# Optimization experiments

Hardware: AMD Instinct MI355X
Metric: run time of the kernel (lower is better)

## Reference

```python
import jax, jax.numpy as jnp
import numpy as np

COMMIT = 0.25
DECAY = 0.999
EPS = 1e-05


def setup_inputs() -> dict:
    key = jax.random.key(0)
    k1, k2, k3, k4 = jax.random.split(key, 4)
    N, M, D = 8, 512, 32
    B, H, W = 32, 32, 32
    return {
        "x": jax.random.normal(k1, (B, N * D, H, W), jnp.float32),
        "embedding": jax.random.uniform(k2, (N, M, D), jnp.float32, -1.0 / M, 1.0 / M),
        "ema_count": jax.random.uniform(k3, (N, M), jnp.float32),
        "ema_weight": jax.random.normal(k4, (N, M, D), jnp.float32) * (1.0 / M),
    }


def reference(x, embedding, ema_count, ema_weight):
    B, C, H, W = x.shape
    N, M, D = embedding.shape  # C == N * D
    xr = x.reshape(B, N, D, H, W).transpose(1, 0, 3, 4, 2)  # [N,B,H,W,D]
    L = B * H * W
    x_flat = jax.lax.stop_gradient(xr).reshape(N, L, D)  # [N,L,D]

    e2 = jnp.sum(embedding ** 2, axis=2)[:, None, :]          # [N,1,M]
    x2 = jnp.sum(x_flat ** 2, axis=2, keepdims=True)          # [N,L,1]
    distances = e2 + x2 - 2.0 * jnp.einsum('nld,nmd->nlm', x_flat, embedding)

    indices = jnp.argmin(distances, axis=-1)                  # [N,L]
    quantized = jnp.take_along_axis(embedding, indices[:, :, None], axis=1)  # [N,L,D]
    quantized = jax.lax.stop_gradient(quantized).reshape(xr.shape)

    # one-hot count / encodings^T @ x_flat expressed as scatter-adds
    n_idx = jnp.arange(N)[:, None]
    counts = jnp.zeros((N, M), x.dtype).at[n_idx, indices].add(1.0)         # [N,M]
    dw = jnp.zeros((N, M, D), x.dtype).at[n_idx, indices].add(x_flat)       # [N,M,D]

    # EMA codebook update (training branch)
    ema_count_new = DECAY * ema_count + (1.0 - DECAY) * counts
    n_tot = jnp.sum(ema_count_new, axis=-1, keepdims=True)
    ema_count_new = (ema_count_new + EPS) / (n_tot + M * EPS) * n_tot
    ema_weight_new = DECAY * ema_weight + (1.0 - DECAY) * dw
    embedding_new = ema_weight_new / ema_count_new[..., None]

    e_latent_loss = jnp.mean((xr - quantized) ** 2)
    loss = COMMIT * e_latent_loss

    quantized_st = xr + jax.lax.stop_gradient(quantized - xr)  # straight-through
    out = quantized_st.transpose(1, 0, 4, 2, 3).reshape(B, C, H, W)

    avg_probs = counts / L                                     # mean of one-hot encodings
    perplexity = jnp.exp(-jnp.sum(avg_probs * jnp.log(avg_probs + 1e-10), axis=-1))

    return out, loss, perplexity.sum(), embedding_new, ema_count_new, ema_weight_new
```

## Files before the change

kernel.cpp:

```cpp
#include <hip/hip_runtime.h>
#include <cfloat>
#include <cmath>

#define NB 32
#define NN 8
#define NM 512
#define ND 32
#define NHW 1024
#define NC 256
#define NCHW (NC * NHW)
#define NL (NB * NHW)
#define EPAD 40
#define XPAD 33

static constexpr float DECAYF = (float)0.999;
static constexpr float OMDF = (float)(1.0 - 0.999);
static constexpr float EPSF = 1e-5f;
static constexpr float MEPSF = (float)(512.0 * 1e-5);
static constexpr float LOSS_SCALE = (float)(0.25 / 8388608.0);

#define OUT_LOSS (NB * NC * NHW)
#define OUT_PERP (OUT_LOSS + 1)
#define OUT_EMB (OUT_PERP + 1)
#define OUT_CNT (OUT_EMB + NN * NM * ND)
#define OUT_W (OUT_CNT + NN * NM)

typedef __attribute__((ext_vector_type(8))) short bf16x8;
typedef __attribute__((ext_vector_type(4))) float f32x4;

__device__ inline unsigned short f2bf(float f) {
    unsigned u = __builtin_bit_cast(unsigned, f);
    u += 0x7FFFu + ((u >> 16) & 1u);
    return (unsigned short)(u >> 16);
}
__device__ inline float bf2f(unsigned short h) {
    unsigned u = ((unsigned)h) << 16;
    return __builtin_bit_cast(float, u);
}

__global__ void e_prep(const float* __restrict__ emb, unsigned short* __restrict__ ehi,
                       unsigned short* __restrict__ elo, float* __restrict__ e2) {
    const int i = blockIdx.x * 256 + threadIdx.x;
    const float* e = emb + i * ND;
    unsigned short* hi = ehi + (size_t)i * EPAD;
    unsigned short* lo = elo + (size_t)i * EPAD;
    float s = 0.f;
#pragma unroll
    for (int d = 0; d < ND; ++d) {
        const float v = e[d];
        s = fmaf(v, v, s);
        const unsigned short h = f2bf(v);
        hi[d] = h;
        lo[d] = f2bf(v - bf2f(h));
    }
    e2[i] = s;
}

__launch_bounds__(256, 2)
__global__ void vq_argmin(const float* __restrict__ x,
                          const unsigned short* __restrict__ ehi,
                          const unsigned short* __restrict__ elo,
                          const float* __restrict__ e2g,
                          const float* __restrict__ emb,
                          float* __restrict__ out,
                          unsigned short* __restrict__ idx_out,
                          float* __restrict__ loss_out) {
    __shared__ __align__(16) unsigned short shi[256 * EPAD];
    __shared__ __align__(16) unsigned short slo[256 * EPAD];
    __shared__ float se2[NM];
    __shared__ __align__(16) float sx[256 * XPAD];
    __shared__ unsigned short sidx[256];
    __shared__ float red[4];

    const int n = blockIdx.y;
    const int lbase = blockIdx.x * 256;
    const int tid = threadIdx.x;
    const int b = lbase >> 10;
    const int hw0 = lbase & (NHW - 1);

    {
        const float* xp = x + (size_t)b * NCHW + n * ND * NHW + hw0 + tid;
#pragma unroll
        for (int d = 0; d < ND; ++d)
            sx[tid * XPAD + d] = xp[d * NHW];
    }
    for (int i = tid; i < NM; i += 256) se2[i] = e2g[n * NM + i];
    __syncthreads();

    const int lane = tid & 63;
    const int w = tid >> 6;
    const int j16 = lane & 15;
    const int kg = lane >> 4;

    bf16x8 ah[4], al[4];
#pragma unroll
    for (int lt = 0; lt < 4; ++lt) {
        const int row = w * 64 + lt * 16 + j16;
        const float* sr = &sx[row * XPAD + kg * 8];
#pragma unroll
        for (int j = 0; j < 8; ++j) {
            const float v = sr[j];
            const unsigned short h = f2bf(v);
            ah[lt][j] = (short)h;
            al[lt][j] = (short)f2bf(v - bf2f(h));
        }
    }

    float bd[4][4];
    int bm[4][4];
#pragma unroll
    for (int lt = 0; lt < 4; ++lt)
#pragma unroll
        for (int r = 0; r < 4; ++r) { bd[lt][r] = FLT_MAX; bm[lt][r] = 0; }

    for (int half = 0; half < 2; ++half) {
        __syncthreads();
        {
            const unsigned* srch = (const unsigned*)(ehi + ((size_t)n * NM + half * 256) * EPAD);
            const unsigned* srcl = (const unsigned*)(elo + ((size_t)n * NM + half * 256) * EPAD);
            unsigned* dsth = (unsigned*)shi;
            unsigned* dstl = (unsigned*)slo;
            for (int i = tid; i < 256 * EPAD / 2; i += 256) {
                dsth[i] = srch[i];
                dstl[i] = srcl[i];
            }
        }
        __syncthreads();

        for (int mt = 0; mt < 16; ++mt) {
            const int mloc = mt * 16 + j16;
            const bf16x8 bh = *(const bf16x8*)&shi[mloc * EPAD + kg * 8];
            const bf16x8 bl = *(const bf16x8*)&slo[mloc * EPAD + kg * 8];
            const int mglob = half * 256 + mloc;
            const float e2v = se2[mglob];
#pragma unroll
            for (int lt = 0; lt < 4; ++lt) {
                f32x4 c = {0.f, 0.f, 0.f, 0.f};
                c = __builtin_amdgcn_mfma_f32_16x16x32_bf16(ah[lt], bh, c, 0, 0, 0);
                c = __builtin_amdgcn_mfma_f32_16x16x32_bf16(al[lt], bh, c, 0, 0, 0);
                c = __builtin_amdgcn_mfma_f32_16x16x32_bf16(ah[lt], bl, c, 0, 0, 0);
#pragma unroll
                for (int r = 0; r < 4; ++r) {
                    const float dist = fmaf(-2.f, c[r], e2v);
                    if (dist < bd[lt][r]) { bd[lt][r] = dist; bm[lt][r] = mglob; }
                }
            }
        }
    }

#pragma unroll
    for (int lt = 0; lt < 4; ++lt)
#pragma unroll
        for (int r = 0; r < 4; ++r) {
            float d0 = bd[lt][r];
            int m0 = bm[lt][r];
#pragma unroll
            for (int off = 1; off < 16; off <<= 1) {
                const float dn = __shfl_xor(d0, off, 64);
                const int mn = __shfl_xor(m0, off, 64);
                if (dn < d0 || (dn == d0 && mn < m0)) { d0 = dn; m0 = mn; }
            }
            bd[lt][r] = d0;
            bm[lt][r] = m0;
        }
    if (j16 == 0) {
#pragma unroll
        for (int lt = 0; lt < 4; ++lt)
#pragma unroll
            for (int r = 0; r < 4; ++r)
                sidx[w * 64 + lt * 16 + kg * 4 + r] = (unsigned short)bm[lt][r];
    }
    __syncthreads();

    const unsigned m = sidx[tid];
    idx_out[n * NL + lbase + tid] = (unsigned short)m;
    const float* q = emb + ((size_t)n * NM + m) * ND;
    float* op = out + (size_t)b * NCHW + n * ND * NHW + hw0 + tid;
    float lacc = 0.f;
#pragma unroll
    for (int d0 = 0; d0 < ND; d0 += 4) {
        const float4 qv = *(const float4*)&q[d0];
        float xd, df;
        xd = sx[tid * XPAD + d0 + 0]; op[(d0 + 0) * NHW] = qv.x; df = xd - qv.x; lacc = fmaf(df, df, lacc);
        xd = sx[tid * XPAD + d0 + 1]; op[(d0 + 1) * NHW] = qv.y; df = xd - qv.y; lacc = fmaf(df, df, lacc);
        xd = sx[tid * XPAD + d0 + 2]; op[(d0 + 2) * NHW] = qv.z; df = xd - qv.z; lacc = fmaf(df, df, lacc);
        xd = sx[tid * XPAD + d0 + 3]; op[(d0 + 3) * NHW] = qv.w; df = xd - qv.w; lacc = fmaf(df, df, lacc);
    }
#pragma unroll
    for (int off = 32; off; off >>= 1) lacc += __shfl_down(lacc, off);
    if (lane == 0) red[w] = lacc;
    __syncthreads();
    if (tid == 0)
        atomicAdd(loss_out, (red[0] + red[1] + red[2] + red[3]) * LOSS_SCALE);
}

__launch_bounds__(256, 2)
__global__ void vq_scatter(const float* __restrict__ x,
                           const unsigned short* __restrict__ idx,
                           float* __restrict__ dw, float* __restrict__ counts) {
    __shared__ float sdw[NM * XPAD];
    __shared__ float scnt[NM];
    const int n = blockIdx.y;
    const int b = blockIdx.x;
    const int tid = threadIdx.x;
    for (int i = tid; i < NM * XPAD; i += 256) sdw[i] = 0.f;
    for (int i = tid; i < NM; i += 256) scnt[i] = 0.f;
    __syncthreads();

    const float* xp = x + (size_t)b * NCHW + n * ND * NHW;
#pragma unroll
    for (int it = 0; it < 4; ++it) {
        const int hw = it * 256 + tid;
        const unsigned m = idx[n * NL + b * NHW + hw];
        float* dst = &sdw[m * XPAD];
#pragma unroll
        for (int d = 0; d < ND; ++d)
            atomicAdd(&dst[d], xp[d * NHW + hw]);
        atomicAdd(&scnt[m], 1.0f);
    }
    __syncthreads();

    float* dwn = dw + (size_t)n * NM * ND;
    for (int i = tid; i < NM * ND; i += 256)
        atomicAdd(&dwn[i], sdw[(i >> 5) * XPAD + (i & 31)]);
    float* cn = counts + n * NM;
    for (int i = tid; i < NM; i += 256) atomicAdd(&cn[i], scnt[i]);
}

__global__ void vq_update_cnt(const float* __restrict__ ema_count,
                              const float* __restrict__ counts,
                              float* __restrict__ out_cnt,
                              float* __restrict__ perp_out) {
    const int n = blockIdx.x;
    const int m = threadIdx.x;
    __shared__ float r1[8], r2[8];
    __shared__ float s_ntot;

    const float cnt = counts[n * NM + m];
    const float cnew = DECAYF * ema_count[n * NM + m] + OMDF * cnt;
    const float avg = cnt / (float)NL;
    const float pterm = avg * logf(avg + 1e-10f);

    float v1 = cnew, v2 = pterm;
#pragma unroll
    for (int off = 32; off; off >>= 1) {
        v1 += __shfl_down(v1, off);
        v2 += __shfl_down(v2, off);
    }
    if ((m & 63) == 0) { r1[m >> 6] = v1; r2[m >> 6] = v2; }
    __syncthreads();
    if (m == 0) {
        float a = 0.f, bsum = 0.f;
#pragma unroll
        for (int i = 0; i < 8; ++i) { a += r1[i]; bsum += r2[i]; }
        s_ntot = a;
        atomicAdd(perp_out, expf(-bsum));
    }
    __syncthreads();
    const float ntot = s_ntot;
    out_cnt[n * NM + m] = (cnew + EPSF) / (ntot + MEPSF) * ntot;
}

__global__ void vq_update_w(const float* __restrict__ ema_weight,
                            const float* __restrict__ dw,
                            const float* __restrict__ out_cnt,
                            float* __restrict__ out_w,
                            float* __restrict__ out_emb) {
    const int i = blockIdx.x * 256 + threadIdx.x;
    const float wnew = DECAYF * ema_weight[i] + OMDF * dw[i];
    out_w[i] = wnew;
    out_emb[i] = wnew / out_cnt[i >> 5];
}

extern "C" void kernel_launch(void* const* d_in, const int* in_sizes, int n_in,
                              void* d_out, int out_size, void* d_ws, size_t ws_size,
                              hipStream_t stream) {
    const float* x = (const float*)d_in[0];
    const float* emb = (const float*)d_in[1];
    const float* ema_count = (const float*)d_in[2];
    const float* ema_weight = (const float*)d_in[3];
    float* out = (float*)d_out;
    char* ws = (char*)d_ws;
    float* ws_f = (float*)d_ws;

    float* counts = ws_f;
    float* dw = ws_f + 4096;
    float* e2 = ws_f + 135168;
    unsigned short* ehi = (unsigned short*)(ws + 557056);
    unsigned short* elo = (unsigned short*)(ws + 884736);
    unsigned short* idxp = (unsigned short*)(ws + 1212416);

    hipMemsetAsync(counts, 0, (size_t)(NN * NM + NN * NM * ND) * sizeof(float), stream);
    hipMemsetAsync(out + OUT_LOSS, 0, 2 * sizeof(float), stream);

    e_prep<<<16, 256, 0, stream>>>(emb, ehi, elo, e2);
    vq_argmin<<<dim3(NL / 256, NN), 256, 0, stream>>>(x, ehi, elo, e2, emb, out, idxp,
                                                      out + OUT_LOSS);
    vq_scatter<<<dim3(NB, NN), 256, 0, stream>>>(x, idxp, dw, counts);
    vq_update_cnt<<<NN, NM, 0, stream>>>(ema_count, counts, out + OUT_CNT, out + OUT_PERP);
    vq_update_w<<<NN * NM * ND / 256, 256, 0, stream>>>(ema_weight, dw, out + OUT_CNT,
                                                        out + OUT_EMB, out + OUT_W);
}
```

Baseline: 207.9 us.

## Stream codebook fragments from global memory and widen scatter blocks

The argmin kernel no longer stages the bf16 hi/lo codebook halves in shared memory. Each lane now loads its MFMA B fragments straight from global/L2 with a one-step register prefetch, which removes two block barriers per half and about 40KB of LDS. That lets the launch bound ask for 4 blocks per CU. The scatter kernel moves to 512-thread blocks so each thread handles fewer pixels, at the cost of more register pressure and global loads that may be less coalesced than the old LDS path.

After: 197.9 us. 4.8% less time.

```diff
diff --git a/kernel.cpp b/kernel.cpp
--- a/kernel.cpp
+++ b/kernel.cpp
@@ -56,7 +56,7 @@
     e2[i] = s;
 }
 
-__launch_bounds__(256, 2)
+__launch_bounds__(256, 4)
 __global__ void vq_argmin(const float* __restrict__ x,
                           const unsigned short* __restrict__ ehi,
                           const unsigned short* __restrict__ elo,
@@ -65,10 +65,8 @@
                           float* __restrict__ out,
                           unsigned short* __restrict__ idx_out,
                           float* __restrict__ loss_out) {
-    __shared__ __align__(16) unsigned short shi[256 * EPAD];
-    __shared__ __align__(16) unsigned short slo[256 * EPAD];
+    __shared__ __align__(16) float sx[256 * XPAD];
     __shared__ float se2[NM];
-    __shared__ __align__(16) float sx[256 * XPAD];
     __shared__ unsigned short sidx[256];
     __shared__ float red[4];
 
@@ -113,37 +111,29 @@
 #pragma unroll
         for (int r = 0; r < 4; ++r) { bd[lt][r] = FLT_MAX; bm[lt][r] = 0; }
 
-    for (int half = 0; half < 2; ++half) {
-        __syncthreads();
-        {
-            const unsigned* srch = (const unsigned*)(ehi + ((size_t)n * NM + half * 256) * EPAD);
-            const unsigned* srcl = (const unsigned*)(elo + ((size_t)n * NM + half * 256) * EPAD);
-            unsigned* dsth = (unsigned*)shi;
-            unsigned* dstl = (unsigned*)slo;
-            for (int i = tid; i < 256 * EPAD / 2; i += 256) {
-                dsth[i] = srch[i];
-                dstl[i] = srcl[i];
-            }
-        }
-        __syncthreads();
-
-        for (int mt = 0; mt < 16; ++mt) {
-            const int mloc = mt * 16 + j16;
-            const bf16x8 bh = *(const bf16x8*)&shi[mloc * EPAD + kg * 8];
-            const bf16x8 bl = *(const bf16x8*)&slo[mloc * EPAD + kg * 8];
-            const int mglob = half * 256 + mloc;
-            const float e2v = se2[mglob];
-#pragma unroll
-            for (int lt = 0; lt < 4; ++lt) {
-                f32x4 c = {0.f, 0.f, 0.f, 0.f};
-                c = __builtin_amdgcn_mfma_f32_16x16x32_bf16(ah[lt], bh, c, 0, 0, 0);
-                c = __builtin_amdgcn_mfma_f32_16x16x32_bf16(al[lt], bh, c, 0, 0, 0);
-                c = __builtin_amdgcn_mfma_f32_16x16x32_bf16(ah[lt], bl, c, 0, 0, 0);
-#pragma unroll
-                for (int r = 0; r < 4; ++r) {
-                    const float dist = fmaf(-2.f, c[r], e2v);
-                    if (dist < bd[lt][r]) { bd[lt][r] = dist; bm[lt][r] = mglob; }
-                }
+    const unsigned short* bh_base = ehi + ((size_t)n * NM + j16) * EPAD + kg * 8;
+    const unsigned short* bl_base = elo + ((size_t)n * NM + j16) * EPAD + kg * 8;
+
+    bf16x8 bh = *(const bf16x8*)(bh_base);
+    bf16x8 bl = *(const bf16x8*)(bl_base);
+    for (int mt = 0; mt < 32; ++mt) {
+        const bf16x8 cbh = bh, cbl = bl;
+        if (mt < 31) {
+            bh = *(const bf16x8*)(bh_base + (size_t)(mt + 1) * 16 * EPAD);
+            bl = *(const bf16x8*)(bl_base + (size_t)(mt + 1) * 16 * EPAD);
+        }
+        const int mloc = mt * 16 + j16;
+        const float e2v = se2[mloc];
+#pragma unroll
+        for (int lt = 0; lt < 4; ++lt) {
+            f32x4 c = {0.f, 0.f, 0.f, 0.f};
+            c = __builtin_amdgcn_mfma_f32_16x16x32_bf16(ah[lt], cbh, c, 0, 0, 0);
+            c = __builtin_amdgcn_mfma_f32_16x16x32_bf16(al[lt], cbh, c, 0, 0, 0);
+            c = __builtin_amdgcn_mfma_f32_16x16x32_bf16(ah[lt], cbl, c, 0, 0, 0);
+#pragma unroll
+            for (int r = 0; r < 4; ++r) {
+                const float dist = fmaf(-2.f, c[r], e2v);
+                if (dist < bd[lt][r]) { bd[lt][r] = dist; bm[lt][r] = mloc; }
             }
         }
     }
@@ -194,7 +184,7 @@
         atomicAdd(loss_out, (red[0] + red[1] + red[2] + red[3]) * LOSS_SCALE);
 }
 
-__launch_bounds__(256, 2)
+__launch_bounds__(512, 2)
 __global__ void vq_scatter(const float* __restrict__ x,
                            const unsigned short* __restrict__ idx,
                            float* __restrict__ dw, float* __restrict__ counts) {
@@ -203,14 +193,15 @@
     const int n = blockIdx.y;
     const int b = blockIdx.x;
     const int tid = threadIdx.x;
-    for (int i = tid; i < NM * XPAD; i += 256) sdw[i] = 0.f;
-    for (int i = tid; i < NM; i += 256) scnt[i] = 0.f;
+
+    for (int i = tid; i < NM * XPAD; i += 512) sdw[i] = 0.f;
+    if (tid < NM) scnt[tid] = 0.f;
     __syncthreads();
 
     const float* xp = x + (size_t)b * NCHW + n * ND * NHW;
 #pragma unroll
-    for (int it = 0; it < 4; ++it) {
-        const int hw = it * 256 + tid;
+    for (int it = 0; it < 2; ++it) {
+        const int hw = it * 512 + tid;
         const unsigned m = idx[n * NL + b * NHW + hw];
         float* dst = &sdw[m * XPAD];
 #pragma unroll
@@ -221,10 +212,9 @@
     __syncthreads();
 
     float* dwn = dw + (size_t)n * NM * ND;
-    for (int i = tid; i < NM * ND; i += 256)
+    for (int i = tid; i < NM * ND; i += 512)
         atomicAdd(&dwn[i], sdw[(i >> 5) * XPAD + (i & 31)]);
-    float* cn = counts + n * NM;
-    for (int i = tid; i < NM; i += 256) atomicAdd(&cn[i], scnt[i]);
+    if (tid < NM) atomicAdd(&counts[n * NM + tid], scnt[tid]);
 }
 
 __global__ void vq_update_cnt(const float* __restrict__ ema_count,
@@ -296,7 +286,7 @@
     e_prep<<<16, 256, 0, stream>>>(emb, ehi, elo, e2);
     vq_argmin<<<dim3(NL / 256, NN), 256, 0, stream>>>(x, ehi, elo, e2, emb, out, idxp,
                                                       out + OUT_LOSS);
-    vq_scatter<<<dim3(NB, NN), 256, 0, stream>>>(x, idxp, dw, counts);
+    vq_scatter<<<dim3(NB, NN), 512, 0, stream>>>(x, idxp, dw, counts);
     vq_update_cnt<<<NN, NM, 0, stream>>>(ema_count, counts, out + OUT_CNT, out + OUT_PERP);
     vq_update_w<<<NN * NM * ND / 256, 256, 0, stream>>>(ema_weight, dw, out + OUT_CNT,
                                                         out + OUT_EMB, out + OUT_W);
```
